# Optimization experiments

Hardware: AMD Instinct MI355X
Metric: run time of the kernel (lower is better)

The kernel has to match this reference:

```python
import jax, jax.numpy as jnp
import numpy as np

D_EMB = 1024
N_HEAD = 16
D_K = D_EMB // N_HEAD


def setup_inputs() -> dict:
    key = jax.random.key(0)
    ks = jax.random.split(key, 11)
    B, S = 2, 2048
    s = 1.0 / np.sqrt(D_EMB)
    inp = {
        'Q': jax.random.normal(ks[0], (B, S, D_EMB), jnp.float32),
        'K': jax.random.normal(ks[1], (B, S, D_EMB), jnp.float32),
        'V': jax.random.normal(ks[2], (B, S, D_EMB), jnp.float32),
        'W_Q': jax.random.normal(ks[3], (D_EMB, D_EMB), jnp.float32) * s,
        'b_Q': jax.random.normal(ks[4], (D_EMB,), jnp.float32) * s,
        'W_K': jax.random.normal(ks[5], (D_EMB, D_EMB), jnp.float32) * s,
        'b_K': jax.random.normal(ks[6], (D_EMB,), jnp.float32) * s,
        'W_V': jax.random.normal(ks[7], (D_EMB, D_EMB), jnp.float32) * s,
        'b_V': jax.random.normal(ks[8], (D_EMB,), jnp.float32) * s,
        'W_O': jax.random.normal(ks[9], (D_EMB, D_EMB), jnp.float32) * s,
        'b_O': jax.random.normal(ks[10], (D_EMB,), jnp.float32) * s,
    }
    return inp


def _heads(x):
    # [B, S, D] -> [B, H, S, d_k]
    B, S, _ = x.shape
    return x.reshape(B, S, N_HEAD, D_K).transpose(0, 2, 1, 3)


def reference(Q, K, V, W_Q, b_Q, W_K, b_K, W_V, b_V, W_O, b_O):
    q = _heads(Q @ W_Q.T + b_Q)
    k = _heads(K @ W_K.T + b_K)
    v = _heads(V @ W_V.T + b_V)
    scale = 1.0 / jnp.sqrt(jnp.asarray(D_K, q.dtype))
    scores = jnp.einsum('bhqd,bhkd->bhqk', q, k) * scale  # [B,H,S,S]
    probs = jax.nn.softmax(scores, axis=-1)
    attn = jnp.einsum('bhqk,bhkd->bhqd', probs, v)
    B, H, S, d = attn.shape
    attn = attn.transpose(0, 2, 1, 3).reshape(B, S, H * d)
    return attn @ W_O.T + b_O
```

## Files before the change

### kernel.cpp

```cpp
#include <hip/hip_runtime.h>
#include <cstdint>
#include <cstddef>

#define S_LEN 2048
#define NH    16
#define DKH   64
#define DEMB  1024
#define MTOT  4096

typedef float f32x4 __attribute__((ext_vector_type(4)));
typedef __bf16 bf16x8 __attribute__((ext_vector_type(8)));
typedef _Float16 f16;
typedef f16 f16x2 __attribute__((ext_vector_type(2)));
typedef f16 f16x4 __attribute__((ext_vector_type(4)));
typedef f16 f16x8 __attribute__((ext_vector_type(8)));
typedef unsigned short u16;
typedef unsigned int u32;
typedef u16 u16x8 __attribute__((ext_vector_type(8)));
typedef u16 u16x4 __attribute__((ext_vector_type(4)));
typedef u32 u32x4 __attribute__((ext_vector_type(4)));

static __device__ __forceinline__ u16 f2bf(float f) {
  u32 u = __builtin_bit_cast(u32, f);
  u += 0x7fffu + ((u >> 16) & 1u);
  return (u16)(u >> 16);
}
static __device__ __forceinline__ float bf2f(u16 b) {
  return __builtin_bit_cast(float, ((u32)b) << 16);
}
static __device__ __forceinline__ bf16x8 ldfrag(const u16* p) {
  return __builtin_bit_cast(bf16x8, *(const u16x8*)p);
}
static __device__ __forceinline__ f16x8 ldfragh8(const u16* p) {
  return __builtin_bit_cast(f16x8, *(const u16x8*)p);
}
static __device__ __forceinline__ f32x4 mfma16(bf16x8 a, bf16x8 b, f32x4 c) {
  return __builtin_amdgcn_mfma_f32_16x16x32_bf16(a, b, c, 0, 0, 0);
}
static __device__ __forceinline__ f32x4 mfmah32(f16x8 a, f16x8 b, f32x4 c) {
  return __builtin_amdgcn_mfma_f32_16x16x32_f16(a, b, c, 0, 0, 0);
}
static __device__ __forceinline__ void gl2lds16(const void* g, void* l) {
  __builtin_amdgcn_global_load_lds((__attribute__((address_space(1))) void*)g,
                                   (__attribute__((address_space(3))) void*)l,
                                   16, 0, 0);
}
static __device__ __forceinline__ u32 pkh2(float a, float b) {
  return __builtin_bit_cast(u32, __builtin_amdgcn_cvt_pkrtz(a, b));
}
static __device__ __forceinline__ f16x4 pkh4(float a, float b, float c, float d) {
  f16x2 lo = __builtin_bit_cast(f16x2, __builtin_amdgcn_cvt_pkrtz(a, b));
  f16x2 hi = __builtin_bit_cast(f16x2, __builtin_amdgcn_cvt_pkrtz(c, d));
  return __builtin_shufflevector(lo, hi, 0, 1, 2, 3);
}

#define SCL_Q (0.125f * 1.44269504088896340736f)

__global__ __launch_bounds__(256) void cvt_w(
    const float* __restrict__ wq, const float* __restrict__ wk,
    const float* __restrict__ wv, const float* __restrict__ wo,
    u16* __restrict__ dW) {
  const int b = blockIdx.x;
  const int seg = b >> 10;
  const float* s = (seg == 0) ? wq : (seg == 1) ? wk : (seg == 2) ? wv : wo;
  u16* d = dW + (size_t)seg * (DEMB * DEMB);
  const int i = ((b & 1023) * 256 + threadIdx.x) * 4;
  f32x4 f = *(const f32x4*)(s + i);
  u16x4 o;
  o[0] = f2bf(f[0]); o[1] = f2bf(f[1]); o[2] = f2bf(f[2]); o[3] = f2bf(f[3]);
  *(u16x4*)(d + i) = o;
}

__global__ __launch_bounds__(256) void qkv_gemm(
    const float* __restrict__ qf, const float* __restrict__ kf,
    const float* __restrict__ vf, const u16* __restrict__ W,
    const float* __restrict__ bq, const float* __restrict__ bk,
    const float* __restrict__ bv,
    u16* __restrict__ qh, u16* __restrict__ kh, u16* __restrict__ vt) {
  __shared__ __align__(16) float sA0[128 * 32], sA1[128 * 32];
  __shared__ __align__(16) u16 sB0[128 * 32], sB1[128 * 32];
  const int t = threadIdx.x;
  const int l = t & 63, w = t >> 6;
  const int ll = l & 15, lg = l >> 4;
  const int orig = blockIdx.x + 24 * blockIdx.y;
  const int xcd = orig & 7, q = orig >> 3;
  const int nb = q >> 2;
  const int mb = xcd * 4 + (q & 3);
  const int which = nb >> 3;
  const float* A = (which == 0) ? qf : ((which == 1) ? kf : vf);
  const int wr = (w >> 1) * 64, wc = (w & 1) * 64;

  f32x4 acc[4][4] = {};

  auto stgA = [&](int kt, float* dA) {
    const int k0 = kt * 32;
#pragma unroll
    for (int i = 0; i < 4; ++i) {
      const int c = i * 256 + t;
      const int row = c >> 3;
      const int gc = (c & 7) ^ (row & 7);
      gl2lds16(A + (size_t)(mb * 128 + row) * DEMB + k0 + gc * 4, &dA[c * 4]);
    }
  };
  auto stgB = [&](int kt, u16* dB) {
    const int k0 = kt * 32;
#pragma unroll
    for (int i = 0; i < 2; ++i) {
      const int c = i * 256 + t;
      const int row = c >> 2;
      const int gc = (c & 3) ^ ((row >> 1) & 3);
      gl2lds16(W + (size_t)(nb * 128 + row) * DEMB + k0 + gc * 8, dB + c * 8);
    }
  };

  auto comp = [&](const float* cA, const u16* cB) {
    bf16x8 af[4], bfr[4];
#pragma unroll
    for (int i2 = 0; i2 < 4; ++i2) {
      const int row = wr + i2 * 16 + ll;
      const f32x4 x0 = *(const f32x4*)&cA[row * 32 + ((2 * lg) ^ (row & 7)) * 4];
      const f32x4 x1 = *(const f32x4*)&cA[row * 32 + ((2 * lg + 1) ^ (row & 7)) * 4];
      u16x8 o;
      o[0] = f2bf(x0[0]); o[1] = f2bf(x0[1]);
      o[2] = f2bf(x0[2]); o[3] = f2bf(x0[3]);
      o[4] = f2bf(x1[0]); o[5] = f2bf(x1[1]);
      o[6] = f2bf(x1[2]); o[7] = f2bf(x1[3]);
      af[i2] = __builtin_bit_cast(bf16x8, o);
    }
#pragma unroll
    for (int j2 = 0; j2 < 4; ++j2) {
      const int row = wc + j2 * 16 + ll;
      bfr[j2] = ldfrag(&cB[row * 32 + (lg ^ ((row >> 1) & 3)) * 8]);
    }
#pragma unroll
    for (int i2 = 0; i2 < 4; ++i2)
#pragma unroll
      for (int j2 = 0; j2 < 4; ++j2)
        acc[i2][j2] = mfma16(af[i2], bfr[j2], acc[i2][j2]);
  };

  stgA(0, sA0); stgB(0, sB0);
  __syncthreads();
  for (int kt2 = 0; kt2 < 16; ++kt2) {
    stgA(2 * kt2 + 1, sA1); stgB(2 * kt2 + 1, sB1);
    comp(sA0, sB0);
    __syncthreads();
    if (kt2 < 15) { stgA(2 * kt2 + 2, sA0); stgB(2 * kt2 + 2, sB0); }
    comp(sA1, sB1);
    __syncthreads();
  }

  const float* bias = (which == 0) ? bq : ((which == 1) ? bk : bv);
  const int b = (mb * 128) >> 11;

  if (which == 2) {
#pragma unroll
    for (int j2 = 0; j2 < 4; ++j2) {
      const int nl = (nb * 128 + wc + j2 * 16 + ll) & 1023;
      const int h = nl >> 6, dk = nl & 63;
      const float bb = bias[nl];
      u16* base = vt + ((size_t)((b * NH + h) * DKH + dk)) * S_LEN;
#pragma unroll
      for (int i2 = 0; i2 < 4; ++i2) {
        const int s = (mb * 128 + wr + i2 * 16 + lg * 4) & 2047;
        const f16x4 pk = pkh4(acc[i2][j2][0] + bb, acc[i2][j2][1] + bb,
                              acc[i2][j2][2] + bb, acc[i2][j2][3] + bb);
        *(u16x4*)&base[s] = __builtin_bit_cast(u16x4, pk);
      }
    }
  } else {
    u16* outp = (which == 0) ? qh : kh;
    const float scl = (which == 0) ? SCL_Q : 1.0f;
#pragma unroll
    for (int j2 = 0; j2 < 4; ++j2) {
      const int nl = (nb * 128 + wc + j2 * 16 + ll) & 1023;
      const int h = nl >> 6, dk = nl & 63;
      const float bb = bias[nl];
#pragma unroll
      for (int i2 = 0; i2 < 4; ++i2) {
#pragma unroll
        for (int r = 0; r < 4; ++r) {
          const int s = (mb * 128 + wr + i2 * 16 + lg * 4 + r) & 2047;
          const float val = (acc[i2][j2][r] + bb) * scl;
          outp[((size_t)((b * NH + h) * S_LEN + s)) * DKH + dk] = f2bf(val);
        }
      }
    }
  }
}

__global__ __launch_bounds__(512, 4) void attn_kernel(
    const u16* __restrict__ qh, const u16* __restrict__ kh,
    const u16* __restrict__ vt, u16* __restrict__ opart,
    float* __restrict__ lpart) {
  __shared__ __align__(16) u16 sK0[64 * 64], sK1[64 * 64];
  __shared__ __align__(16) u16 sV0[64 * 64], sV1[64 * 64];
  const int t = threadIdx.x;
  const int l = t & 63, w = t >> 6;
  const int ll = l & 15, lg = l >> 4;
  const int qb = blockIdx.x >> 1;
  const int ks = blockIdx.x & 1;
  const int q_blk = qb * 256;
  const int bh = blockIdx.y;

  bf16x8 aq[2][2];
#pragma unroll
  for (int qt = 0; qt < 2; ++qt) {
    const u16* qbase =
        qh + ((size_t)bh * S_LEN + q_blk + w * 32 + qt * 16 + ll) * DKH;
    aq[qt][0] = ldfrag(qbase + lg * 8);
    aq[qt][1] = ldfrag(qbase + 32 + lg * 8);
  }

  f32x4 oT[2][4] = {};
  float l_part[2] = {0.f, 0.f};

  const int strow = t >> 3;
  const int sgc = (t & 7) ^ (strow & 7);
  const u16* kstg =
      kh + ((size_t)bh * S_LEN + ks * 1024 + strow) * DKH + sgc * 8;
  const u16* vstg =
      vt + ((size_t)bh * DKH + strow) * S_LEN + ks * 1024 + sgc * 8;

  auto stg = [&](int kt, u16* dK, u16* dV) {
    gl2lds16(kstg + (size_t)kt * 64 * DKH, dK + t * 8);
    gl2lds16(vstg + kt * 64, dV + t * 8);
  };

  auto compute = [&](const u16* cK, const u16* cV) {
#pragma unroll
    for (int pr = 0; pr < 2; ++pr) {
      u32 pw0[4], pw1[4];
#pragma unroll
      for (int h = 0; h < 2; ++h) {
        const int krow = (pr * 2 + h) * 16 + ll;
        const bf16x8 ak0 = ldfrag(&cK[krow * 64 + (lg ^ (ll & 7)) * 8]);
        const bf16x8 ak1 = ldfrag(&cK[krow * 64 + ((4 + lg) ^ (ll & 7)) * 8]);
        f32x4 s0 = {}, s1 = {};
        s0 = mfma16(ak0, aq[0][0], s0);
        s0 = mfma16(ak1, aq[0][1], s0);
        s1 = mfma16(ak0, aq[1][0], s1);
        s1 = mfma16(ak1, aq[1][1], s1);
        {
          const float p0 = __builtin_amdgcn_exp2f(s0[0]);
          const float p1 = __builtin_amdgcn_exp2f(s0[1]);
          const float p2 = __builtin_amdgcn_exp2f(s0[2]);
          const float p3 = __builtin_amdgcn_exp2f(s0[3]);
          l_part[0] += (p0 + p1) + (p2 + p3);
          if (h == 0) { pw0[0] = pkh2(p0, p1); pw0[1] = pkh2(p2, p3); }
          else        { pw0[2] = pkh2(p0, p1); pw0[3] = pkh2(p2, p3); }
        }
        {
          const float p0 = __builtin_amdgcn_exp2f(s1[0]);
          const float p1 = __builtin_amdgcn_exp2f(s1[1]);
          const float p2 = __builtin_amdgcn_exp2f(s1[2]);
          const float p3 = __builtin_amdgcn_exp2f(s1[3]);
          l_part[1] += (p0 + p1) + (p2 + p3);
          if (h == 0) { pw1[0] = pkh2(p0, p1); pw1[1] = pkh2(p2, p3); }
          else        { pw1[2] = pkh2(p0, p1); pw1[3] = pkh2(p2, p3); }
        }
      }
      asm volatile("v_permlane32_swap_b32 %0, %1" : "+v"(pw0[0]), "+v"(pw0[2]));
      asm volatile("v_permlane16_swap_b32 %0, %1" : "+v"(pw0[0]), "+v"(pw0[2]));
      asm volatile("v_permlane32_swap_b32 %0, %1" : "+v"(pw0[1]), "+v"(pw0[3]));
      asm volatile("v_permlane16_swap_b32 %0, %1" : "+v"(pw0[1]), "+v"(pw0[3]));
      asm volatile("v_permlane32_swap_b32 %0, %1" : "+v"(pw1[0]), "+v"(pw1[2]));
      asm volatile("v_permlane16_swap_b32 %0, %1" : "+v"(pw1[0]), "+v"(pw1[2]));
      asm volatile("v_permlane32_swap_b32 %0, %1" : "+v"(pw1[1]), "+v"(pw1[3]));
      asm volatile("v_permlane16_swap_b32 %0, %1" : "+v"(pw1[1]), "+v"(pw1[3]));
      const f16x8 bp0 =
          __builtin_bit_cast(f16x8, (u32x4){pw0[0], pw0[1], pw0[2], pw0[3]});
      const f16x8 bp1 =
          __builtin_bit_cast(f16x8, (u32x4){pw1[0], pw1[1], pw1[2], pw1[3]});

#pragma unroll
      for (int nt = 0; nt < 4; ++nt) {
        const int row = nt * 16 + ll;
        const f16x8 av =
            ldfragh8(&cV[row * 64 + ((pr * 4 + lg) ^ (ll & 7)) * 8]);
        oT[0][nt] = mfmah32(av, bp0, oT[0][nt]);
        oT[1][nt] = mfmah32(av, bp1, oT[1][nt]);
      }
    }
  };

  stg(0, sK0, sV0);
  __syncthreads();
  for (int kt2 = 0; kt2 < 8; ++kt2) {
    stg(2 * kt2 + 1, sK1, sV1);
    compute(sK0, sV0);
    __syncthreads();
    if (kt2 < 7) stg(2 * kt2 + 2, sK0, sV0);
    compute(sK1, sV1);
    __syncthreads();
  }

#pragma unroll
  for (int qt = 0; qt < 2; ++qt) {
    float lv = l_part[qt];
    lv += __shfl_xor(lv, 16, 64);
    lv += __shfl_xor(lv, 32, 64);
    const int orow = q_blk + w * 32 + qt * 16 + ll;
    u16* obase = opart + (((size_t)(ks * 32 + bh)) * S_LEN + orow) * DKH;
#pragma unroll
    for (int nt = 0; nt < 4; ++nt) {
      u16x4 o;
#pragma unroll
      for (int r = 0; r < 4; ++r) o[r] = f2bf(oT[qt][nt][r]);
      *(u16x4*)&obase[nt * 16 + lg * 4] = o;
    }
    if (lg == 0) lpart[(ks * 32 + bh) * S_LEN + orow] = lv;
  }
}

__global__ __launch_bounds__(256) void merge_ctx(
    const u16* __restrict__ op, const float* __restrict__ lp,
    u16* __restrict__ ctx) {
  const int idx = blockIdx.x * 256 + threadIdx.x;
  const int dk8 = idx & 7;
  const int q = (idx >> 3) & 2047;
  const int bh = idx >> 14;
  const float inv = 1.0f / (lp[bh * S_LEN + q] + lp[(32 + bh) * S_LEN + q]);
  const u16x8 a = *(const u16x8*)&op[((size_t)bh * S_LEN + q) * DKH + dk8 * 8];
  const u16x8 c = *(const u16x8*)&op[((size_t)(32 + bh) * S_LEN + q) * DKH + dk8 * 8];
  u16x8 o;
#pragma unroll
  for (int r = 0; r < 8; ++r) o[r] = f2bf((bf2f(a[r]) + bf2f(c[r])) * inv);
  const int b = bh >> 4, h = bh & 15;
  *(u16x8*)&ctx[((size_t)((b * S_LEN + q) * NH + h)) * DKH + dk8 * 8] = o;
}

__global__ __launch_bounds__(256) void out_gemm(
    const u16* __restrict__ Am, const u16* __restrict__ W,
    const float* __restrict__ bo, float* __restrict__ out) {
  __shared__ __align__(16) u16 sA0[128 * 64], sA1[128 * 64];
  __shared__ __align__(16) u16 sB0[64 * 64], sB1[64 * 64];
  const int t = threadIdx.x;
  const int l = t & 63, w = t >> 6;
  const int ll = l & 15, lg = l >> 4;
  const int nb = blockIdx.x;
  const int mb = blockIdx.y;
  const int wr = (w >> 1) * 64, wc = (w & 1) * 32;

  f32x4 acc[4][2] = {};

  auto stg = [&](int kt, u16* dA, u16* dB) {
    const int k0 = kt * 64;
#pragma unroll
    for (int i = 0; i < 4; ++i) {
      const int c = i * 256 + t;
      const int row = c >> 3;
      const int gc = (c & 7) ^ (row & 7);
      gl2lds16(Am + (size_t)(mb * 128 + row) * DEMB + k0 + gc * 8, dA + c * 8);
      if (i < 2)
        gl2lds16(W + (size_t)(nb * 64 + row) * DEMB + k0 + gc * 8, dB + c * 8);
    }
  };

  auto comp = [&](const u16* cA, const u16* cB) {
#pragma unroll
    for (int kk = 0; kk < 2; ++kk) {
      bf16x8 af[4], bfr[2];
#pragma unroll
      for (int i2 = 0; i2 < 4; ++i2) {
        const int row = wr + i2 * 16 + ll;
        af[i2] = ldfrag(&cA[row * 64 + ((kk * 4 + lg) ^ (row & 7)) * 8]);
      }
#pragma unroll
      for (int j2 = 0; j2 < 2; ++j2) {
        const int row = wc + j2 * 16 + ll;
        bfr[j2] = ldfrag(&cB[row * 64 + ((kk * 4 + lg) ^ (row & 7)) * 8]);
      }
#pragma unroll
      for (int i2 = 0; i2 < 4; ++i2)
#pragma unroll
        for (int j2 = 0; j2 < 2; ++j2)
          acc[i2][j2] = mfma16(af[i2], bfr[j2], acc[i2][j2]);
    }
  };

  stg(0, sA0, sB0);
  __syncthreads();
  for (int kt2 = 0; kt2 < 8; ++kt2) {
    stg(2 * kt2 + 1, sA1, sB1);
    comp(sA0, sB0);
    __syncthreads();
    if (kt2 < 7) stg(2 * kt2 + 2, sA0, sB0);
    comp(sA1, sB1);
    __syncthreads();
  }

#pragma unroll
  for (int j2 = 0; j2 < 2; ++j2) {
    const int ncol = nb * 64 + wc + j2 * 16 + ll;
    const float bb = bo[ncol];
#pragma unroll
    for (int i2 = 0; i2 < 4; ++i2) {
#pragma unroll
      for (int r = 0; r < 4; ++r) {
        const int mrow = mb * 128 + wr + i2 * 16 + lg * 4 + r;
        out[(size_t)mrow * DEMB + ncol] = acc[i2][j2][r] + bb;
      }
    }
  }
}

extern "C" void kernel_launch(void* const* d_in, const int* in_sizes, int n_in,
                              void* d_out, int out_size, void* d_ws,
                              size_t ws_size, hipStream_t stream) {
  (void)in_sizes; (void)n_in; (void)out_size; (void)ws_size;
  const float* Q  = (const float*)d_in[0];
  const float* K  = (const float*)d_in[1];
  const float* V  = (const float*)d_in[2];
  const float* WQ = (const float*)d_in[3];
  const float* bQ = (const float*)d_in[4];
  const float* WK = (const float*)d_in[5];
  const float* bK = (const float*)d_in[6];
  const float* WV = (const float*)d_in[7];
  const float* bV = (const float*)d_in[8];
  const float* WO = (const float*)d_in[9];
  const float* bO = (const float*)d_in[10];
  float* out = (float*)d_out;

  u16* ws   = (u16*)d_ws;
  u16* Wqkv = ws;
  u16* Wo   = Wqkv + (size_t)3072 * 1024;
  u16* qh   = Wo + (size_t)1024 * 1024;
  u16* kh   = qh + (size_t)32 * 2048 * 64;
  u16* vt   = kh + (size_t)32 * 2048 * 64;
  u16* ctx  = vt + (size_t)32 * 2048 * 64;
  u16* opart   = ctx + (size_t)MTOT * DEMB;
  float* lpart = (float*)(opart + (size_t)2 * 32 * 2048 * 64);

  cvt_w<<<4096, 256, 0, stream>>>(WQ, WK, WV, WO, Wqkv);
  qkv_gemm<<<dim3(24, 32), 256, 0, stream>>>(Q, K, V, Wqkv, bQ, bK, bV,
                                             qh, kh, vt);
  attn_kernel<<<dim3(16, 32), 512, 0, stream>>>(qh, kh, vt, opart, lpart);
  merge_ctx<<<2048, 256, 0, stream>>>(opart, lpart, ctx);
  out_gemm<<<dim3(16, 32), 256, 0, stream>>>(ctx, Wo, bO, out);
}
```

Before: 222.8 us.

## Fuse split-K attention merge into output projection GEMM A-tile load

Removes the separate merge_ctx kernel. The output GEMM now reads both split-K partial attention outputs directly into shared memory and combines them with the precomputed reciprocal denominators while building its A fragments. The K tile is halved to 32 so each step covers half of one head. This saves a kernel launch plus the write and re-read of the ctx buffer, but it doubles A-tile traffic in the GEMM, which is repeated across all 16 N-blocks, and adds conversion ALU work inside the MFMA loop.

```diff
diff --git a/kernel.cpp b/kernel.cpp
--- a/kernel.cpp
+++ b/kernel.cpp
@@ -7,6 +7,7 @@
 #define DKH   64
 #define DEMB  1024
 #define MTOT  4096
+#define SLAB  ((size_t)32 * S_LEN * DKH)
 
 typedef float f32x4 __attribute__((ext_vector_type(4)));
 typedef __bf16 bf16x8 __attribute__((ext_vector_type(8)));
@@ -30,6 +31,9 @@
 }
 static __device__ __forceinline__ bf16x8 ldfrag(const u16* p) {
   return __builtin_bit_cast(bf16x8, *(const u16x8*)p);
+}
+static __device__ __forceinline__ u16x8 ldu16x8(const u16* p) {
+  return *(const u16x8*)p;
 }
 static __device__ __forceinline__ f16x8 ldfragh8(const u16* p) {
   return __builtin_bit_cast(f16x8, *(const u16x8*)p);
@@ -313,80 +317,89 @@
   }
 }
 
-__global__ __launch_bounds__(256) void merge_ctx(
+__global__ __launch_bounds__(256) void out_gemm(
     const u16* __restrict__ op, const float* __restrict__ lp,
-    u16* __restrict__ ctx) {
-  const int idx = blockIdx.x * 256 + threadIdx.x;
-  const int dk8 = idx & 7;
-  const int q = (idx >> 3) & 2047;
-  const int bh = idx >> 14;
-  const float inv = 1.0f / (lp[bh * S_LEN + q] + lp[(32 + bh) * S_LEN + q]);
-  const u16x8 a = *(const u16x8*)&op[((size_t)bh * S_LEN + q) * DKH + dk8 * 8];
-  const u16x8 c = *(const u16x8*)&op[((size_t)(32 + bh) * S_LEN + q) * DKH + dk8 * 8];
-  u16x8 o;
-#pragma unroll
-  for (int r = 0; r < 8; ++r) o[r] = f2bf((bf2f(a[r]) + bf2f(c[r])) * inv);
-  const int b = bh >> 4, h = bh & 15;
-  *(u16x8*)&ctx[((size_t)((b * S_LEN + q) * NH + h)) * DKH + dk8 * 8] = o;
-}
-
-__global__ __launch_bounds__(256) void out_gemm(
-    const u16* __restrict__ Am, const u16* __restrict__ W,
-    const float* __restrict__ bo, float* __restrict__ out) {
-  __shared__ __align__(16) u16 sA0[128 * 64], sA1[128 * 64];
-  __shared__ __align__(16) u16 sB0[64 * 64], sB1[64 * 64];
+    const u16* __restrict__ W, const float* __restrict__ bo,
+    float* __restrict__ out) {
+  __shared__ __align__(16) u16 sA0a[128 * 32], sA0b[128 * 32];
+  __shared__ __align__(16) u16 sA1a[128 * 32], sA1b[128 * 32];
+  __shared__ __align__(16) u16 sB0[64 * 32], sB1[64 * 32];
+  __shared__ float sInv[128 * 17];
   const int t = threadIdx.x;
   const int l = t & 63, w = t >> 6;
   const int ll = l & 15, lg = l >> 4;
   const int nb = blockIdx.x;
   const int mb = blockIdx.y;
   const int wr = (w >> 1) * 64, wc = (w & 1) * 32;
+  const int b = mb >> 4;
+  const int s0 = (mb * 128) & 2047;
+
+  for (int e = t; e < 128 * 16; e += 256) {
+    const int row = e >> 4, h = e & 15;
+    const float l0 = lp[(size_t)(b * 16 + h) * S_LEN + s0 + row];
+    const float l1 = lp[(size_t)(32 + b * 16 + h) * S_LEN + s0 + row];
+    sInv[row * 17 + h] = 1.0f / (l0 + l1);
+  }
 
   f32x4 acc[4][2] = {};
 
-  auto stg = [&](int kt, u16* dA, u16* dB) {
-    const int k0 = kt * 64;
-#pragma unroll
-    for (int i = 0; i < 4; ++i) {
+  auto stg = [&](int kt, u16* dAa, u16* dAb, u16* dB) {
+    const int h = kt >> 1, kd = (kt & 1) * 32;
+#pragma unroll
+    for (int i = 0; i < 2; ++i) {
       const int c = i * 256 + t;
-      const int row = c >> 3;
-      const int gc = (c & 7) ^ (row & 7);
-      gl2lds16(Am + (size_t)(mb * 128 + row) * DEMB + k0 + gc * 8, dA + c * 8);
-      if (i < 2)
-        gl2lds16(W + (size_t)(nb * 64 + row) * DEMB + k0 + gc * 8, dB + c * 8);
-    }
-  };
-
-  auto comp = [&](const u16* cA, const u16* cB) {
-#pragma unroll
-    for (int kk = 0; kk < 2; ++kk) {
-      bf16x8 af[4], bfr[2];
-#pragma unroll
-      for (int i2 = 0; i2 < 4; ++i2) {
-        const int row = wr + i2 * 16 + ll;
-        af[i2] = ldfrag(&cA[row * 64 + ((kk * 4 + lg) ^ (row & 7)) * 8]);
-      }
-#pragma unroll
-      for (int j2 = 0; j2 < 2; ++j2) {
-        const int row = wc + j2 * 16 + ll;
-        bfr[j2] = ldfrag(&cB[row * 64 + ((kk * 4 + lg) ^ (row & 7)) * 8]);
-      }
-#pragma unroll
-      for (int i2 = 0; i2 < 4; ++i2)
-#pragma unroll
-        for (int j2 = 0; j2 < 2; ++j2)
-          acc[i2][j2] = mfma16(af[i2], bfr[j2], acc[i2][j2]);
-    }
-  };
-
-  stg(0, sA0, sB0);
+      const int row = c >> 2;
+      const int gc = (c & 3) ^ ((row >> 1) & 3);
+      const size_t src =
+          ((size_t)(b * 16 + h) * S_LEN + s0 + row) * DKH + kd + gc * 8;
+      gl2lds16(op + src, dAa + c * 8);
+      gl2lds16(op + SLAB + src, dAb + c * 8);
+    }
+    {
+      const int c = t;
+      const int row = c >> 2;
+      const int gc = (c & 3) ^ ((row >> 1) & 3);
+      gl2lds16(W + (size_t)(nb * 64 + row) * DEMB + h * 64 + kd + gc * 8,
+               dB + c * 8);
+    }
+  };
+
+  auto comp = [&](const u16* cAa, const u16* cAb, const u16* cB, int kt) {
+    const int h = kt >> 1;
+    bf16x8 af[4], bfr[2];
+#pragma unroll
+    for (int i2 = 0; i2 < 4; ++i2) {
+      const int row = wr + i2 * 16 + ll;
+      const int ch = (lg ^ ((row >> 1) & 3)) * 8;
+      const u16x8 a0 = ldu16x8(&cAa[row * 32 + ch]);
+      const u16x8 a1 = ldu16x8(&cAb[row * 32 + ch]);
+      const float inv = sInv[row * 17 + h];
+      u16x8 o;
+#pragma unroll
+      for (int e = 0; e < 8; ++e)
+        o[e] = f2bf((bf2f(a0[e]) + bf2f(a1[e])) * inv);
+      af[i2] = __builtin_bit_cast(bf16x8, o);
+    }
+#pragma unroll
+    for (int j2 = 0; j2 < 2; ++j2) {
+      const int row = wc + j2 * 16 + ll;
+      bfr[j2] = ldfrag(&cB[row * 32 + (lg ^ ((row >> 1) & 3)) * 8]);
+    }
+#pragma unroll
+    for (int i2 = 0; i2 < 4; ++i2)
+#pragma unroll
+      for (int j2 = 0; j2 < 2; ++j2)
+        acc[i2][j2] = mfma16(af[i2], bfr[j2], acc[i2][j2]);
+  };
+
+  stg(0, sA0a, sA0b, sB0);
   __syncthreads();
-  for (int kt2 = 0; kt2 < 8; ++kt2) {
-    stg(2 * kt2 + 1, sA1, sB1);
-    comp(sA0, sB0);
-    __syncthreads();
-    if (kt2 < 7) stg(2 * kt2 + 2, sA0, sB0);
-    comp(sA1, sB1);
+  for (int kt2 = 0; kt2 < 16; ++kt2) {
+    stg(2 * kt2 + 1, sA1a, sA1b, sB1);
+    comp(sA0a, sA0b, sB0, 2 * kt2);
+    __syncthreads();
+    if (kt2 < 15) stg(2 * kt2 + 2, sA0a, sA0b, sB0);
+    comp(sA1a, sA1b, sB1, 2 * kt2 + 1);
     __syncthreads();
   }
 
@@ -428,14 +441,12 @@
   u16* qh   = Wo + (size_t)1024 * 1024;
   u16* kh   = qh + (size_t)32 * 2048 * 64;
   u16* vt   = kh + (size_t)32 * 2048 * 64;
-  u16* ctx  = vt + (size_t)32 * 2048 * 64;
-  u16* opart   = ctx + (size_t)MTOT * DEMB;
-  float* lpart = (float*)(opart + (size_t)2 * 32 * 2048 * 64);
+  u16* opart   = vt + (size_t)32 * 2048 * 64;
+  float* lpart = (float*)(opart + 2 * SLAB);
 
   cvt_w<<<4096, 256, 0, stream>>>(WQ, WK, WV, WO, Wqkv);
   qkv_gemm<<<dim3(24, 32), 256, 0, stream>>>(Q, K, V, Wqkv, bQ, bK, bV,
                                              qh, kh, vt);
   attn_kernel<<<dim3(16, 32), 512, 0, stream>>>(qh, kh, vt, opart, lpart);
-  merge_ctx<<<2048, 256, 0, stream>>>(opart, lpart, ctx);
-  out_gemm<<<dim3(16, 32), 256, 0, stream>>>(ctx, Wo, bO, out);
-}
+  out_gemm<<<dim3(16, 32), 256, 0, stream>>>(opart, lpart, Wo, bO, out);
+}
```

After: 243.5 us. 9.3% more time.
